# Kernel optimization log

Measured on AMD Instinct MI355X. Metric: run time of the kernel, lower is better.

The kernel has to match this reference:

```python
import jax, jax.numpy as jnp
import numpy as np

B, T, E, A = 4, 4096, 256, 64

def setup_inputs() -> dict:
    key = jax.random.key(0)
    ks = jax.random.split(key, 7)
    s = 1.0 / np.sqrt(E)
    return {
        "embedded": jax.random.normal(ks[0], (B, T, E), dtype=jnp.float32),
        "Wk": jax.random.normal(ks[1], (E, A), dtype=jnp.float32) * s,
        "bk": jax.random.normal(ks[2], (A,), dtype=jnp.float32) * s,
        "Wq": jax.random.normal(ks[3], (E, A), dtype=jnp.float32) * s,
        "bq": jax.random.normal(ks[4], (A,), dtype=jnp.float32) * s,
        "Wv": jax.random.normal(ks[5], (E, A), dtype=jnp.float32) * s,
        "bv": jax.random.normal(ks[6], (A,), dtype=jnp.float32) * s,
    }

def reference(embedded, Wk, bk, Wq, bq, Wv, bv):
    k = embedded @ Wk + bk                      # [B,T,A]
    q = embedded @ Wq + bq
    v = embedded @ Wv + bv
    scale = 1.0 / jnp.sqrt(jnp.asarray(k.shape[-1], dtype=k.dtype))
    scores = jnp.einsum('bqa,bka->bqk', q, k) * scale   # [B,T,T]
    Tn = scores.shape[-1]
    causal = jnp.tril(jnp.ones((Tn, Tn), dtype=bool))
    scores = jnp.where(causal, scores, -jnp.inf)
    sm = jax.nn.softmax(scores, axis=-1)
    return jnp.einsum('bqk,bka->bqa', sm, v)            # [B,T,A]
```

## Files before the change

kernel.cpp:

```cpp
#include <hip/hip_runtime.h>
#include <math.h>

#define Bn 4
#define Tn 4096
#define En 256
#define An 64
#define PLS 72
#define WLS 264

typedef __attribute__((ext_vector_type(8))) short short8;
typedef __attribute__((ext_vector_type(8))) __bf16 bf16x8;
typedef __attribute__((ext_vector_type(4))) float f32x4;
typedef __attribute__((ext_vector_type(4))) short short4v;
typedef __attribute__((ext_vector_type(2))) unsigned int uint2v;

__device__ __forceinline__ f32x4 mfma16(short8 a, short8 b, f32x4 c) {
    return __builtin_amdgcn_mfma_f32_16x16x32_bf16(
        __builtin_bit_cast(bf16x8, a), __builtin_bit_cast(bf16x8, b), c, 0, 0, 0);
}
__device__ __forceinline__ unsigned short f2bf(float x) {
    return __builtin_bit_cast(unsigned short, (__bf16)x);
}
__device__ __forceinline__ float bf2f(unsigned short h) {
    return __builtin_bit_cast(float, (unsigned int)h << 16);
}
__device__ __forceinline__ unsigned int packbf2(float lo, float hi) {
    return (unsigned int)f2bf(lo) | ((unsigned int)f2bf(hi) << 16);
}

__global__ __launch_bounds__(256, 2) void proj_kernel(
    const float* __restrict__ emb,
    const float* __restrict__ Wq, const float* __restrict__ Wk, const float* __restrict__ Wv,
    const float* __restrict__ bq, const float* __restrict__ bk, const float* __restrict__ bv,
    unsigned short* __restrict__ qg, unsigned short* __restrict__ kg,
    unsigned short* __restrict__ v_t)
{
    const int bid  = blockIdx.x;
    const int tid  = threadIdx.x;
    const int wave = tid >> 6, lane = tid & 63, quad = lane >> 4, l15 = lane & 15;
    const int jh   = bid & 1;
    const int rb   = bid >> 1;
    const int row0  = rb * 64;
    const int b     = row0 >> 12;
    const int trow0 = row0 & 4095;

    __shared__ unsigned short Wl[96 * WLS];
    __shared__ unsigned short vtr[64 * PLS];

    {
        const float* __restrict__ srcA = jh ? Wv : Wq;
        const int lrbA = jh ? 32 : 0;
#pragma unroll
        for (int it = 0; it < 16; it++) {
            const int idx = it * 256 + tid;
            const int col = idx & 63;
            const int e0  = (idx >> 6) * 4;
            const float w0 = srcA[(size_t)(e0 + 0) * An + col];
            const float w1 = srcA[(size_t)(e0 + 1) * An + col];
            const float w2 = srcA[(size_t)(e0 + 2) * An + col];
            const float w3 = srcA[(size_t)(e0 + 3) * An + col];
            *(short4v*)&Wl[(lrbA + col) * WLS + e0] =
                (short4v){(short)f2bf(w0), (short)f2bf(w1), (short)f2bf(w2), (short)f2bf(w3)};
        }
        const int coloff = jh ? 32 : 0;
        const int lrbB   = jh ? 0 : 64;
#pragma unroll
        for (int it = 0; it < 8; it++) {
            const int idx = it * 256 + tid;
            const int col = idx & 31;
            const int e0  = (idx >> 5) * 4;
            const float w0 = Wk[(size_t)(e0 + 0) * An + coloff + col];
            const float w1 = Wk[(size_t)(e0 + 1) * An + coloff + col];
            const float w2 = Wk[(size_t)(e0 + 2) * An + coloff + col];
            const float w3 = Wk[(size_t)(e0 + 3) * An + coloff + col];
            *(short4v*)&Wl[(lrbB + col) * WLS + e0] =
                (short4v){(short)f2bf(w0), (short)f2bf(w1), (short)f2bf(w2), (short)f2bf(w3)};
        }
    }

    short8 A[8];
    {
        const float* erow = emb + (size_t)(row0 + wave * 16 + l15) * En;
#pragma unroll
        for (int c = 0; c < 8; c++) {
            const float* pp = erow + c * 32 + quad * 8;
            float4 f0 = *(const float4*)pp;
            float4 f1 = *(const float4*)(pp + 4);
            A[c] = (short8){(short)f2bf(f0.x), (short)f2bf(f0.y), (short)f2bf(f0.z), (short)f2bf(f0.w),
                            (short)f2bf(f1.x), (short)f2bf(f1.y), (short)f2bf(f1.z), (short)f2bf(f1.w)};
        }
    }
    __syncthreads();

    f32x4 acc[6];
#pragma unroll
    for (int x = 0; x < 6; x++) acc[x] = (f32x4){0.f, 0.f, 0.f, 0.f};

#pragma unroll
    for (int x = 0; x < 6; x++) {
        const unsigned short* wrow = &Wl[(x * 16 + l15) * WLS];
#pragma unroll
        for (int c = 0; c < 8; c++)
            acc[x] = mfma16(A[c], *(const short8*)(wrow + c * 32 + quad * 8), acc[x]);
    }

    const float QS = 0.125f * 1.4426950408889634f;
#pragma unroll
    for (int x = 0; x < 6; x++) {
        const int nt = jh * 6 + x;
        const int m  = nt >> 2;
        const int al = (nt & 3) * 16 + l15;
        const float bsv = ((m == 0) ? bq : (m == 1) ? bk : bv)[al];
#pragma unroll
        for (int rg = 0; rg < 4; rg++) {
            const int row_l = wave * 16 + quad * 4 + rg;
            const float val = acc[x][rg] + bsv;
            if (m == 0)      qg[(size_t)(row0 + row_l) * An + al] = f2bf(val * QS);
            else if (m == 1) kg[(size_t)(row0 + row_l) * An + al] = f2bf(val);
            else             vtr[al * PLS + row_l] = f2bf(val);
        }
    }
    if (jh == 1) {
        __syncthreads();
        const int a  = tid >> 2;
        const int tg = (tid & 3) * 16;
        unsigned short* dst = v_t + (size_t)(b * 64 + a) * Tn + trow0 + tg;
        *(short8*)dst       = *(const short8*)&vtr[a * PLS + tg];
        *(short8*)(dst + 8) = *(const short8*)&vtr[a * PLS + tg + 8];
    }
}

__global__ __launch_bounds__(256, 2) void flash_kernel(
    const unsigned short* __restrict__ qg, const unsigned short* __restrict__ kg,
    const unsigned short* __restrict__ v_t,
    unsigned short* __restrict__ Opart, float* __restrict__ Lp,
    int S, int lgS)
{
    const int b    = blockIdx.y;
    const int tid  = threadIdx.x;
    const int wave = tid >> 6, lane = tid & 63, quad = lane >> 4, l15 = lane & 15;
    const int ub   = blockIdx.x;
    const int S4   = S >> 2;
    const int p    = ub >> (lgS - 2);
    const int sb   = ub & (S4 - 1);
    const int s    = sb * 4 + wave;

    __shared__ unsigned short lds[4 * 64 * PLS];
    __shared__ float lW[4][64];
    unsigned short* tw = lds + wave * (64 * PLS);

    const unsigned short* kb0 = kg  + ((size_t)b << 12) * An;
    const unsigned short* vb0 = v_t + (size_t)b * An * Tn;

#pragma unroll 1
    for (int tile = 0; tile < 2; tile++) {
        const int qt    = tile ? (63 - p) : p;
        const int qrow0 = qt * 64;
        const int tmax  = qt;

        short8 qB[4][2];
        {
            const unsigned short* qb = qg + (((size_t)b << 12) + qrow0) * An;
#pragma unroll
            for (int g = 0; g < 4; g++)
#pragma unroll
                for (int c = 0; c < 2; c++)
                    qB[g][c] = *(const short8*)(qb + (size_t)(16 * g + l15) * An + c * 32 + quad * 8);
        }

        float lacc[4] = {0.f, 0.f, 0.f, 0.f};
        f32x4 O[4][4];
#pragma unroll
        for (int nt = 0; nt < 4; nt++)
#pragma unroll
            for (int g = 0; g < 4; g++) O[nt][g] = (f32x4){0.f, 0.f, 0.f, 0.f};

        int t = s;
        if (t <= tmax) {
            short8 KA[4][2];
            {
                const unsigned short* kb = kb0 + (size_t)t * (64 * An);
#pragma unroll
                for (int nt = 0; nt < 4; nt++)
#pragma unroll
                    for (int c = 0; c < 2; c++)
                        KA[nt][c] = *(const short8*)(kb + (nt * 16 + l15) * An + c * 32 + quad * 8);
            }
            for (;;) {
                short8 VA[4][2];
                {
                    const unsigned short* vb = vb0 + (size_t)t * 64;
#pragma unroll
                    for (int nt = 0; nt < 4; nt++)
#pragma unroll
                        for (int c = 0; c < 2; c++)
                            VA[nt][c] = *(const short8*)(vb + (size_t)(nt * 16 + l15) * Tn + c * 32 + quad * 8);
                }

                const int tn = t + S;
                const bool more = (tn <= tmax);
                short8 KN[4][2];
                if (more) {
                    const unsigned short* kb = kb0 + (size_t)tn * (64 * An);
#pragma unroll
                    for (int nt = 0; nt < 4; nt++)
#pragma unroll
                        for (int c = 0; c < 2; c++)
                            KN[nt][c] = *(const short8*)(kb + (nt * 16 + l15) * An + c * 32 + quad * 8);
                }

                const bool diag = (t == tmax);

#pragma unroll
                for (int g = 0; g < 4; g++) {
                    f32x4 St[4];
#pragma unroll
                    for (int nt = 0; nt < 4; nt++) {
                        f32x4 a0 = (f32x4){0.f, 0.f, 0.f, 0.f};
                        a0 = mfma16(KA[nt][0], qB[g][0], a0);
                        a0 = mfma16(KA[nt][1], qB[g][1], a0);
                        St[nt] = a0;
                    }
                    if (diag) {
                        const int qr = 16 * g + l15;
                        const int kvb = quad * 4;
#pragma unroll
                        for (int nt = 0; nt < 4; nt++)
#pragma unroll
                            for (int rg = 0; rg < 4; rg++)
                                if (nt * 16 + kvb + rg > qr) St[nt][rg] = -__builtin_inff();
                    }
                    float rs = 0.f;
#pragma unroll
                    for (int nt = 0; nt < 4; nt++) {
                        const float p0 = exp2f(St[nt][0]);
                        const float p1 = exp2f(St[nt][1]);
                        const float p2 = exp2f(St[nt][2]);
                        const float p3 = exp2f(St[nt][3]);
                        rs += (p0 + p1) + (p2 + p3);
                        const unsigned int d0 = packbf2(p0, p1);
                        const unsigned int d1 = packbf2(p2, p3);
                        *(short4v*)&tw[(16 * g + l15) * PLS + 16 * nt + quad * 4] =
                            __builtin_bit_cast(short4v, (uint2v){d0, d1});
                    }
                    lacc[g] += rs;
#pragma unroll
                    for (int c = 0; c < 2; c++) {
                        const short8 pb = *(const short8*)&tw[(16 * g + l15) * PLS + c * 32 + quad * 8];
#pragma unroll
                        for (int nt = 0; nt < 4; nt++)
                            O[nt][g] = mfma16(VA[nt][c], pb, O[nt][g]);
                    }
                }

                if (!more) break;
                t = tn;
#pragma unroll
                for (int nt = 0; nt < 4; nt++)
#pragma unroll
                    for (int c = 0; c < 2; c++) KA[nt][c] = KN[nt][c];
            }
        }

#pragma unroll
        for (int nt = 0; nt < 4; nt++)
#pragma unroll
            for (int g = 0; g < 4; g++) {
                const unsigned int d0 = packbf2(O[nt][g][0], O[nt][g][1]);
                const unsigned int d1 = packbf2(O[nt][g][2], O[nt][g][3]);
                *(short4v*)&tw[(16 * g + l15) * PLS + 16 * nt + quad * 4] =
                    __builtin_bit_cast(short4v, (uint2v){d0, d1});
            }
#pragma unroll
        for (int g = 0; g < 4; g++) {
            lacc[g] += __shfl_xor(lacc[g], 16);
            lacc[g] += __shfl_xor(lacc[g], 32);
        }
        if (quad == 0) {
#pragma unroll
            for (int g = 0; g < 4; g++) lW[wave][16 * g + l15] = lacc[g];
        }
        __syncthreads();

        {
            const int row = tid >> 2;
            const int a16 = (tid & 3) * 16;
            float acc[16];
#pragma unroll
            for (int x = 0; x < 16; x++) acc[x] = 0.f;
            float lsum = 0.f;
#pragma unroll
            for (int w = 0; w < 4; w++) {
                const unsigned short* src = lds + w * (64 * PLS) + row * PLS + a16;
                const short8 o0 = *(const short8*)src;
                const short8 o1 = *(const short8*)(src + 8);
#pragma unroll
                for (int x = 0; x < 8; x++) {
                    acc[x]     += bf2f((unsigned short)o0[x]);
                    acc[8 + x] += bf2f((unsigned short)o1[x]);
                }
                lsum += lW[w][row];
            }
            const size_t unit = (size_t)(b * 64 + qt) * (size_t)S4 + sb;
            unsigned short* ob = Opart + unit * 4096 + row * 64 + a16;
            short8 r0, r1;
#pragma unroll
            for (int x = 0; x < 8; x++) {
                r0[x] = (short)f2bf(acc[x]);
                r1[x] = (short)f2bf(acc[8 + x]);
            }
            *(short8*)ob       = r0;
            *(short8*)(ob + 8) = r1;
            if ((tid & 3) == 0) Lp[unit * 64 + row] = lsum;
        }
        __syncthreads();
    }
}

__global__ __launch_bounds__(256) void merge_kernel(
    const unsigned short* __restrict__ Opart, const float* __restrict__ Lp,
    float* __restrict__ out, int S4)
{
    const int qt = blockIdx.x, b = blockIdx.y;
    const int tid = threadIdx.x;
    const int qr  = tid >> 2;
    const int a16 = (tid & 3) * 16;
    const size_t ub = (size_t)(b * 64 + qt) * (size_t)S4;

    float acc[16];
#pragma unroll
    for (int x = 0; x < 16; x++) acc[x] = 0.f;
    float lsum = 0.f;

#pragma unroll 1
    for (int sb = 0; sb < S4; sb++) {
        const unsigned short* op = &Opart[(ub + sb) * 4096 + qr * 64 + a16];
        const short8 o0 = *(const short8*)op;
        const short8 o1 = *(const short8*)(op + 8);
#pragma unroll
        for (int x = 0; x < 8; x++) {
            acc[x]     += bf2f((unsigned short)o0[x]);
            acc[8 + x] += bf2f((unsigned short)o1[x]);
        }
        lsum += Lp[(ub + sb) * 64 + qr];
    }
    const float inv = 1.f / lsum;
    float* o = out + (((size_t)b << 12) + qt * 64 + qr) * An + a16;
#pragma unroll
    for (int h = 0; h < 4; h++) {
        float4 r = {acc[h * 4] * inv, acc[h * 4 + 1] * inv,
                    acc[h * 4 + 2] * inv, acc[h * 4 + 3] * inv};
        *(float4*)(o + h * 4) = r;
    }
}

extern "C" void kernel_launch(void* const* d_in, const int* in_sizes, int n_in,
                              void* d_out, int out_size, void* d_ws, size_t ws_size,
                              hipStream_t stream) {
    const float* emb = (const float*)d_in[0];
    const float* Wk  = (const float*)d_in[1];
    const float* bk  = (const float*)d_in[2];
    const float* Wq  = (const float*)d_in[3];
    const float* bq  = (const float*)d_in[4];
    const float* Wv  = (const float*)d_in[5];
    const float* bv  = (const float*)d_in[6];
    float* out = (float*)d_out;

    char* ws = (char*)d_ws;
    const size_t MB = 1024 * 1024;

    int S = 8, lgS = 3;
    if (7 * MB + (size_t)256 * 8 * 4096 * 2 <= ws_size)      { S = 32; lgS = 5; }
    else if (7 * MB + (size_t)256 * 4 * 4096 * 2 <= ws_size) { S = 16; lgS = 4; }
    const int S4 = S >> 2;

    unsigned short* q     = (unsigned short*)(ws);
    unsigned short* k     = (unsigned short*)(ws + 2 * MB);
    unsigned short* v_t   = (unsigned short*)(ws + 4 * MB);
    float*          Lp    = (float*)(ws + 6 * MB);
    unsigned short* Opart = (unsigned short*)(ws + 7 * MB);

    proj_kernel<<<512, 256, 0, stream>>>(emb, Wq, Wk, Wv, bq, bk, bv, q, k, v_t);
    flash_kernel<<<dim3(8 * S, 4), 256, 0, stream>>>(q, k, v_t, Opart, Lp, S, lgS);
    merge_kernel<<<dim3(64, 4), 256, 0, stream>>>(Opart, Lp, out, S4);
}
```

Baseline: 143.6 us.

## Fuse split-K merge into flash kernel via atomic last-block reduction

Removes the separate merge kernel: each flash block bumps an atomic counter per (batch, query tile), and the last block to finish reduces all partial outputs and writes the final normalized result. It also adds s_setprio around MFMA groups to favour matrix-issue scheduling, and reduces the default split from 32 to 16 when workspace allows. This saves a kernel launch and the global round-trip latency, at the cost of a memset, fences and a serialized tail reduction in the last block per tile. The smaller split lowers parallelism and partial traffic.

Result: slower. 328.6 us (+128.8%).

```diff
diff --git a/kernel.cpp b/kernel.cpp
--- a/kernel.cpp
+++ b/kernel.cpp
@@ -134,6 +134,7 @@
     const unsigned short* __restrict__ qg, const unsigned short* __restrict__ kg,
     const unsigned short* __restrict__ v_t,
     unsigned short* __restrict__ Opart, float* __restrict__ Lp,
+    float* __restrict__ out, unsigned int* __restrict__ cnt,
     int S, int lgS)
 {
     const int b    = blockIdx.y;
@@ -147,6 +148,7 @@
 
     __shared__ unsigned short lds[4 * 64 * PLS];
     __shared__ float lW[4][64];
+    __shared__ int lastw;
     unsigned short* tw = lds + wave * (64 * PLS);
 
     const unsigned short* kb0 = kg  + ((size_t)b << 12) * An;
@@ -214,6 +216,7 @@
 #pragma unroll
                 for (int g = 0; g < 4; g++) {
                     f32x4 St[4];
+                    __builtin_amdgcn_s_setprio(1);
 #pragma unroll
                     for (int nt = 0; nt < 4; nt++) {
                         f32x4 a0 = (f32x4){0.f, 0.f, 0.f, 0.f};
@@ -221,6 +224,7 @@
                         a0 = mfma16(KA[nt][1], qB[g][1], a0);
                         St[nt] = a0;
                     }
+                    __builtin_amdgcn_s_setprio(0);
                     if (diag) {
                         const int qr = 16 * g + l15;
                         const int kvb = quad * 4;
@@ -247,9 +251,11 @@
 #pragma unroll
                     for (int c = 0; c < 2; c++) {
                         const short8 pb = *(const short8*)&tw[(16 * g + l15) * PLS + c * 32 + quad * 8];
+                        __builtin_amdgcn_s_setprio(1);
 #pragma unroll
                         for (int nt = 0; nt < 4; nt++)
                             O[nt][g] = mfma16(VA[nt][c], pb, O[nt][g]);
+                        __builtin_amdgcn_s_setprio(0);
                     }
                 }
 
@@ -313,44 +319,45 @@
             *(short8*)(ob + 8) = r1;
             if ((tid & 3) == 0) Lp[unit * 64 + row] = lsum;
         }
-        __syncthreads();
-    }
-}
-
-__global__ __launch_bounds__(256) void merge_kernel(
-    const unsigned short* __restrict__ Opart, const float* __restrict__ Lp,
-    float* __restrict__ out, int S4)
-{
-    const int qt = blockIdx.x, b = blockIdx.y;
-    const int tid = threadIdx.x;
-    const int qr  = tid >> 2;
-    const int a16 = (tid & 3) * 16;
-    const size_t ub = (size_t)(b * 64 + qt) * (size_t)S4;
-
-    float acc[16];
-#pragma unroll
-    for (int x = 0; x < 16; x++) acc[x] = 0.f;
-    float lsum = 0.f;
-
+
+        __threadfence();
+        __syncthreads();
+        if (tid == 0) {
+            const unsigned int old = atomicAdd(&cnt[b * 64 + qt], 1u);
+            lastw = (old == (unsigned int)(S4 - 1)) ? 1 : 0;
+        }
+        __syncthreads();
+        if (lastw) {
+            __threadfence();
+            const int row = tid >> 2;
+            const int a16 = (tid & 3) * 16;
+            const size_t ubase = (size_t)(b * 64 + qt) * (size_t)S4;
+            float facc[16];
+#pragma unroll
+            for (int x = 0; x < 16; x++) facc[x] = 0.f;
+            float lsum = 0.f;
 #pragma unroll 1
-    for (int sb = 0; sb < S4; sb++) {
-        const unsigned short* op = &Opart[(ub + sb) * 4096 + qr * 64 + a16];
-        const short8 o0 = *(const short8*)op;
-        const short8 o1 = *(const short8*)(op + 8);
-#pragma unroll
-        for (int x = 0; x < 8; x++) {
-            acc[x]     += bf2f((unsigned short)o0[x]);
-            acc[8 + x] += bf2f((unsigned short)o1[x]);
-        }
-        lsum += Lp[(ub + sb) * 64 + qr];
-    }
-    const float inv = 1.f / lsum;
-    float* o = out + (((size_t)b << 12) + qt * 64 + qr) * An + a16;
-#pragma unroll
-    for (int h = 0; h < 4; h++) {
-        float4 r = {acc[h * 4] * inv, acc[h * 4 + 1] * inv,
-                    acc[h * 4 + 2] * inv, acc[h * 4 + 3] * inv};
-        *(float4*)(o + h * 4) = r;
+            for (int sbi = 0; sbi < S4; sbi++) {
+                const unsigned short* op = &Opart[(ubase + sbi) * 4096 + row * 64 + a16];
+                const short8 o0 = *(const short8*)op;
+                const short8 o1 = *(const short8*)(op + 8);
+#pragma unroll
+                for (int x = 0; x < 8; x++) {
+                    facc[x]     += bf2f((unsigned short)o0[x]);
+                    facc[8 + x] += bf2f((unsigned short)o1[x]);
+                }
+                lsum += Lp[(ubase + sbi) * 64 + row];
+            }
+            const float inv = 1.f / lsum;
+            float* o = out + (((size_t)b << 12) + qt * 64 + row) * An + a16;
+#pragma unroll
+            for (int h = 0; h < 4; h++) {
+                float4 r = {facc[h * 4] * inv, facc[h * 4 + 1] * inv,
+                            facc[h * 4 + 2] * inv, facc[h * 4 + 3] * inv};
+                *(float4*)(o + h * 4) = r;
+            }
+        }
+        __syncthreads();
     }
 }
 
@@ -370,17 +377,16 @@
     const size_t MB = 1024 * 1024;
 
     int S = 8, lgS = 3;
-    if (7 * MB + (size_t)256 * 8 * 4096 * 2 <= ws_size)      { S = 32; lgS = 5; }
-    else if (7 * MB + (size_t)256 * 4 * 4096 * 2 <= ws_size) { S = 16; lgS = 4; }
-    const int S4 = S >> 2;
+    if (7 * MB + (size_t)1024 * 8192 <= ws_size) { S = 16; lgS = 4; }
 
     unsigned short* q     = (unsigned short*)(ws);
     unsigned short* k     = (unsigned short*)(ws + 2 * MB);
     unsigned short* v_t   = (unsigned short*)(ws + 4 * MB);
     float*          Lp    = (float*)(ws + 6 * MB);
+    unsigned int*   cnt   = (unsigned int*)(ws + 6 * MB + 512 * 1024);
     unsigned short* Opart = (unsigned short*)(ws + 7 * MB);
 
+    hipMemsetAsync(cnt, 0, 256 * sizeof(unsigned int), stream);
     proj_kernel<<<512, 256, 0, stream>>>(emb, Wq, Wk, Wv, bq, bk, bv, q, k, v_t);
-    flash_kernel<<<dim3(8 * S, 4), 256, 0, stream>>>(q, k, v_t, Opart, Lp, S, lgS);
-    merge_kernel<<<dim3(64, 4), 256, 0, stream>>>(Opart, Lp, out, S4);
-}
+    flash_kernel<<<dim3(8 * S, 4), 256, 0, stream>>>(q, k, v_t, Opart, Lp, out, cnt, S, lgS);
+}
```
